# Kernel optimization log

Hardware: AMD Instinct MI355X
Metric: run time of the kernel (lower is better)

## Reference

```python
import jax, jax.numpy as jnp
import numpy as np

N, T, HID, H = 2, 2048, 1024, 16
D = HID // H


def setup_inputs() -> dict:
    key = jax.random.key(0)
    ks = jax.random.split(key, 11)
    s = 1.0 / np.sqrt(HID)
    return {
        "q": jax.random.normal(ks[0], (N, T, HID), jnp.float32),
        "k": jax.random.normal(ks[1], (N, T, HID), jnp.float32),
        "v": jax.random.normal(ks[2], (N, T, HID), jnp.float32),
        "Wq": jax.random.normal(ks[3], (HID, HID), jnp.float32) * s,
        "bq": jnp.zeros((HID,), jnp.float32),
        "Wk": jax.random.normal(ks[4], (HID, HID), jnp.float32) * s,
        "bk": jnp.zeros((HID,), jnp.float32),
        "Wv": jax.random.normal(ks[5], (HID, HID), jnp.float32) * s,
        "bv": jnp.zeros((HID,), jnp.float32),
        "Wo": jax.random.normal(ks[6], (HID, HID), jnp.float32) * s,
        "bo": jnp.zeros((HID,), jnp.float32),
    }


def reference(q, k, v, Wq, bq, Wk, bk, Wv, bv, Wo, bo):
    n, t, _ = q.shape
    # Linear projections, then the original's quirky head split:
    # .view(N, H, T, D) directly from (N, T, H*D) (no transpose).
    qh = (q @ Wq + bq).reshape(n, H, t, D)
    kh = (k @ Wk + bk).reshape(n, H, t, D)
    vh = (v @ Wv + bv).reshape(n, H, t, D)
    # scores: (N, H, T, T), scaled by sqrt(hidden_size) (not head dim)
    scores = jnp.einsum("nhtd,nhsd->nhts", qh, kh) / jnp.sqrt(jnp.float32(HID))
    # faithful quirk: softmax over dim=1 (the head axis)
    attn = jax.nn.softmax(scores, axis=1)
    # dropout is identity (eval / drop_rate=0)
    out = jnp.einsum("nhts,nhsd->nhtd", attn, vh).reshape(n, t, H * D)
    return out @ Wo + bo
```

## Files before the change

kernel.cpp:

```cpp
#include <hip/hip_runtime.h>

typedef unsigned short u16;
typedef __bf16 bf16x8 __attribute__((ext_vector_type(8)));
typedef float f32x4 __attribute__((ext_vector_type(4)));

#define MFMA16 __builtin_amdgcn_mfma_f32_16x16x32_bf16

constexpr int NB = 2, TS = 2048, HD = 1024, NH = 16, DH = 64;
constexpr float ALPHA = 0.045084220027780106f;

__device__ __forceinline__ u16 f2bf(float f) {
    union { float f; unsigned u; } v; v.f = f;
    unsigned r = v.u + 0x7FFFu + ((v.u >> 16) & 1u);
    return (u16)(r >> 16);
}
__device__ __forceinline__ float bf2f(u16 h) {
    union { unsigned u; float f; } v; v.u = ((unsigned)h) << 16;
    return v.f;
}
__device__ __forceinline__ bf16x8 ldb8(const u16* p) {
    return *reinterpret_cast<const bf16x8*>(p);
}
__device__ __forceinline__ void glds16(const u16* g, u16* l) {
    __builtin_amdgcn_global_load_lds(
        (const __attribute__((address_space(1))) unsigned int*)g,
        (__attribute__((address_space(3))) unsigned int*)l, 16, 0, 0);
}

#if defined(__has_builtin)
#  if __has_builtin(__builtin_amdgcn_cvt_pk_bf16_f32)
#    define HAVE_PKBF16 1
#  endif
#  if __has_builtin(__builtin_amdgcn_exp2f)
#    define HAVE_EXP2 1
#  endif
#endif
#ifndef HAVE_PKBF16
#  define HAVE_PKBF16 0
#endif
#ifndef HAVE_EXP2
#  define HAVE_EXP2 0
#endif
__device__ __forceinline__ unsigned pk2(float a, float b) {
#if HAVE_PKBF16
    typedef __bf16 bf16x2 __attribute__((ext_vector_type(2)));
    bf16x2 r = __builtin_amdgcn_cvt_pk_bf16_f32(a, b);
    return __builtin_bit_cast(unsigned, r);
#else
    return (unsigned)f2bf(a) | ((unsigned)f2bf(b) << 16);
#endif
}
__device__ __forceinline__ float fexp2(float x) {
#if HAVE_EXP2
    return __builtin_amdgcn_exp2f(x);
#else
    return exp2f(x);
#endif
}

__global__ __launch_bounds__(256) void to_bf16(
    const float* __restrict__ a0, const float* __restrict__ a1, const float* __restrict__ a2,
    u16* __restrict__ o0, u16* __restrict__ o1, u16* __restrict__ o2)
{
    const float* s; u16* d;
    if (blockIdx.y == 0)      { s = a0; d = o0; }
    else if (blockIdx.y == 1) { s = a1; d = o1; }
    else                      { s = a2; d = o2; }
    size_t i = ((size_t)blockIdx.x * 256 + threadIdx.x) * 8;
    float4 v0 = *reinterpret_cast<const float4*>(s + i);
    float4 v1 = *reinterpret_cast<const float4*>(s + i + 4);
    uint4 w = { pk2(v0.x, v0.y), pk2(v0.z, v0.w), pk2(v1.x, v1.y), pk2(v1.z, v1.w) };
    *reinterpret_cast<uint4*>(d + i) = w;
}

__global__ __launch_bounds__(256) void wtrans(
    const float* __restrict__ w0, const float* __restrict__ w1,
    const float* __restrict__ w2, const float* __restrict__ w3,
    u16* __restrict__ o0, u16* __restrict__ o1,
    u16* __restrict__ o2, u16* __restrict__ o3)
{
    const float* src; u16* dst; float sc;
    if (blockIdx.z == 0)      { src = w0; dst = o0; sc = ALPHA; }
    else if (blockIdx.z == 1) { src = w1; dst = o1; sc = 1.0f; }
    else if (blockIdx.z == 2) { src = w2; dst = o2; sc = 1.0f; }
    else                      { src = w3; dst = o3; sc = 1.0f; }
    __shared__ __align__(16) u16 tile[64 * 72];
    const int k0 = blockIdx.y * 64, n0 = blockIdx.x * 64;
    const int t = threadIdx.x, r = t >> 2, c0 = (t & 3) << 4;
#pragma unroll
    for (int j = 0; j < 4; ++j) {
        float4 v = *reinterpret_cast<const float4*>(&src[(size_t)(k0 + r) * HD + n0 + c0 + 4 * j]);
        tile[(c0 + 4 * j + 0) * 72 + r] = f2bf(v.x * sc);
        tile[(c0 + 4 * j + 1) * 72 + r] = f2bf(v.y * sc);
        tile[(c0 + 4 * j + 2) * 72 + r] = f2bf(v.z * sc);
        tile[(c0 + 4 * j + 3) * 72 + r] = f2bf(v.w * sc);
    }
    __syncthreads();
#pragma unroll
    for (int j = 0; j < 2; ++j)
        *reinterpret_cast<uint4*>(&dst[(size_t)(n0 + r) * HD + k0 + c0 + 8 * j]) =
            *reinterpret_cast<const uint4*>(&tile[r * 72 + c0 + 8 * j]);
}

__global__ __launch_bounds__(256) void gemm_qkv(
    const u16* __restrict__ A0, const u16* __restrict__ A1, const u16* __restrict__ A2,
    const u16* __restrict__ B0, const u16* __restrict__ B1, const u16* __restrict__ B2,
    const float* __restrict__ c0, const float* __restrict__ c1, const float* __restrict__ c2,
    u16* __restrict__ C0, u16* __restrict__ C1, u16* __restrict__ VT)
{
    const u16 *A, *BT; const float* bias;
    if (blockIdx.z == 0)      { A = A0; BT = B0; bias = c0; }
    else if (blockIdx.z == 1) { A = A1; BT = B1; bias = c1; }
    else                      { A = A2; BT = B2; bias = c2; }
    constexpr int N = HD, K = HD;
    __shared__ __align__(16) u16 As[128 * 32];
    __shared__ __align__(16) u16 Bs[128 * 32];
    const int m0 = blockIdx.y * 128, n0 = blockIdx.x * 128;
    const int tid = threadIdx.x, wid = tid >> 6, lane = tid & 63;
    const int q = lane >> 4, c = lane & 15;
    const int wm = wid >> 1, wn = wid & 1;
    const int srow = tid >> 2, scol = (tid & 3) << 3;
    f32x4 acc[4][4] = {};
    for (int k0 = 0; k0 < K; k0 += 32) {
        glds16(&A[(size_t)(m0 + srow) * K + k0 + scol],       &As[tid * 8]);
        glds16(&A[(size_t)(m0 + 64 + srow) * K + k0 + scol],  &As[2048 + tid * 8]);
        glds16(&BT[(size_t)(n0 + srow) * K + k0 + scol],      &Bs[tid * 8]);
        glds16(&BT[(size_t)(n0 + 64 + srow) * K + k0 + scol], &Bs[2048 + tid * 8]);
        __syncthreads();
        bf16x8 af[4], bf[4];
#pragma unroll
        for (int i = 0; i < 4; ++i)  af[i] = ldb8(&As[(wm * 64 + i * 16 + c) * 32 + q * 8]);
#pragma unroll
        for (int jn = 0; jn < 4; ++jn) bf[jn] = ldb8(&Bs[(wn * 64 + jn * 16 + c) * 32 + q * 8]);
#pragma unroll
        for (int i = 0; i < 4; ++i)
#pragma unroll
            for (int jn = 0; jn < 4; ++jn)
                acc[i][jn] = MFMA16(bf[jn], af[i], acc[i][jn], 0, 0, 0);
        __syncthreads();
    }
    if (blockIdx.z == 2) {
#pragma unroll
        for (int i = 0; i < 4; ++i)
#pragma unroll
            for (int jn = 0; jn < 4; ++jn) {
                int row = m0 + wm * 64 + i * 16 + c;
                int nn = row >> 11, tp = row & 2047;
                int col = n0 + wn * 64 + jn * 16 + q * 4;
                int hh  = tp >> 7;
                int tau = ((tp & 127) << 4) + (col >> 6);
                int d0  = col & 63;
#pragma unroll
                for (int r = 0; r < 4; ++r)
                    VT[(size_t)((nn * 16 + hh) * 64 + d0 + r) * 2048 + tau] =
                        f2bf(acc[i][jn][r] + bias[col + r]);
            }
    } else {
        u16* C = (blockIdx.z == 0) ? C0 : C1;
        const float bsc = (blockIdx.z == 0) ? ALPHA : 1.0f;
#pragma unroll
        for (int i = 0; i < 4; ++i)
#pragma unroll
            for (int jn = 0; jn < 4; ++jn) {
                int row = m0 + wm * 64 + i * 16 + c;
                int col = n0 + wn * 64 + jn * 16 + q * 4;
                float4 bb = *reinterpret_cast<const float4*>(&bias[col]);
                uint2 w = { pk2(acc[i][jn][0] + bb.x * bsc, acc[i][jn][1] + bb.y * bsc),
                            pk2(acc[i][jn][2] + bb.z * bsc, acc[i][jn][3] + bb.w * bsc) };
                *reinterpret_cast<uint2*>(&C[(size_t)row * N + col]) = w;
            }
    }
}

__global__ __launch_bounds__(256) void gemm_out(
    const u16* __restrict__ A, const u16* __restrict__ BT,
    const float* __restrict__ bias, float* __restrict__ C,
    int M, int N, int K)
{
    __shared__ __align__(16) u16 As[64 * 32];
    __shared__ __align__(16) u16 Bs[128 * 32];
    const int m0 = blockIdx.y * 64, n0 = blockIdx.x * 128;
    const int tid = threadIdx.x, wid = tid >> 6, lane = tid & 63;
    const int q = lane >> 4, c = lane & 15;
    const int wm = wid >> 1, wn = wid & 1;
    const int arow = tid >> 2, acol = (tid & 3) << 3;
    f32x4 acc[2][4] = {};
    for (int k0 = 0; k0 < K; k0 += 32) {
        glds16(&A[(size_t)(m0 + arow) * K + k0 + acol], &As[tid * 8]);
        glds16(&BT[(size_t)(n0 + arow) * K + k0 + acol], &Bs[tid * 8]);
        glds16(&BT[(size_t)(n0 + 64 + arow) * K + k0 + acol], &Bs[2048 + tid * 8]);
        __syncthreads();
        bf16x8 af[2], bf[4];
#pragma unroll
        for (int jm = 0; jm < 2; ++jm) af[jm] = ldb8(&As[(wm * 32 + jm * 16 + c) * 32 + q * 8]);
#pragma unroll
        for (int jn = 0; jn < 4; ++jn) bf[jn] = ldb8(&Bs[(wn * 64 + jn * 16 + c) * 32 + q * 8]);
#pragma unroll
        for (int jm = 0; jm < 2; ++jm)
#pragma unroll
            for (int jn = 0; jn < 4; ++jn)
                acc[jm][jn] = MFMA16(bf[jn], af[jm], acc[jm][jn], 0, 0, 0);
        __syncthreads();
    }
#pragma unroll
    for (int jm = 0; jm < 2; ++jm)
#pragma unroll
        for (int jn = 0; jn < 4; ++jn) {
            int row = m0 + wm * 32 + jm * 16 + c;
            int col = n0 + wn * 64 + jn * 16 + q * 4;
            float4 bb = *reinterpret_cast<const float4*>(&bias[col]);
            float4 v = { acc[jm][jn][0] + bb.x, acc[jm][jn][1] + bb.y,
                         acc[jm][jn][2] + bb.z, acc[jm][jn][3] + bb.w };
            *reinterpret_cast<float4*>(&C[(size_t)row * N + col]) = v;
        }
}

__global__ __launch_bounds__(256) void z_kernel(
    const u16* __restrict__ Qp, const u16* __restrict__ Kp, u16* __restrict__ Zf)
{
    __shared__ __align__(16) u16 Ks[64 * 64];
    __shared__ __align__(16) u16 Qs[128 * 64];
    const int sb = blockIdx.x, tb = blockIdx.y, n = blockIdx.z;
    const int s0 = sb * 64, t0 = tb * 128;
    const int tid = threadIdx.x, wid = tid >> 6, lane = tid & 63;
    const int q = lane >> 4, c = lane & 15;
    const int krow = tid >> 3, kch = tid & 7;
    float zacc[2][4][4] = {};
    for (int h = 0; h < NH; ++h) {
        const u16* Qh = Qp + (size_t)(n * NH + h) * TS * DH;
        const u16* Kh = Kp + (size_t)(n * NH + h) * TS * DH;
        glds16(&Kh[(size_t)(s0 + krow) * DH + ((kch ^ (krow & 7)) << 3)], &Ks[tid * 8]);
        glds16(&Kh[(size_t)(s0 + 32 + krow) * DH + ((kch ^ (krow & 7)) << 3)], &Ks[2048 + tid * 8]);
#pragma unroll
        for (int L = 0; L < 4; ++L)
            glds16(&Qh[(size_t)(t0 + L * 32 + krow) * DH + ((kch ^ (krow & 7)) << 3)],
                   &Qs[L * 2048 + tid * 8]);
        __syncthreads();
        bf16x8 qa[2][2], kb[4][2];
#pragma unroll
        for (int jm = 0; jm < 2; ++jm)
#pragma unroll
            for (int kf = 0; kf < 2; ++kf)
                qa[jm][kf] = ldb8(&Qs[(wid * 32 + jm * 16 + c) * 64 + (((kf * 4 + q) ^ (c & 7)) << 3)]);
#pragma unroll
        for (int i = 0; i < 4; ++i)
#pragma unroll
            for (int kf = 0; kf < 2; ++kf)
                kb[i][kf] = ldb8(&Ks[(i * 16 + c) * 64 + (((kf * 4 + q) ^ (c & 7)) << 3)]);
        f32x4 s_[2][4] = {};
#pragma unroll
        for (int kf = 0; kf < 2; ++kf)
#pragma unroll
            for (int jm = 0; jm < 2; ++jm)
#pragma unroll
                for (int i = 0; i < 4; ++i)
                    s_[jm][i] = MFMA16(kb[i][kf], qa[jm][kf], s_[jm][i], 0, 0, 0);
#pragma unroll
        for (int jm = 0; jm < 2; ++jm)
#pragma unroll
            for (int i = 0; i < 4; ++i)
#pragma unroll
                for (int r = 0; r < 4; ++r)
                    zacc[jm][i][r] += fexp2(s_[jm][i][r]);
        __syncthreads();
    }
#pragma unroll
    for (int jm = 0; jm < 2; ++jm) {
        int t = t0 + wid * 32 + jm * 16 + c;
        size_t zb = ((size_t)((n * 32 + sb) * 2048) + t) * 64 + q * 16;
        unsigned w32[8];
#pragma unroll
        for (int i = 0; i < 4; ++i) {
            w32[i * 2 + 0] = pk2(1.0f / zacc[jm][i][0], 1.0f / zacc[jm][i][1]);
            w32[i * 2 + 1] = pk2(1.0f / zacc[jm][i][2], 1.0f / zacc[jm][i][3]);
        }
        *reinterpret_cast<uint4*>(&Zf[zb])     = *reinterpret_cast<const uint4*>(&w32[0]);
        *reinterpret_cast<uint4*>(&Zf[zb + 8]) = *reinterpret_cast<const uint4*>(&w32[4]);
    }
}

__global__ __launch_bounds__(256) void attn_kernel(
    const u16* __restrict__ Qp, const u16* __restrict__ Kp, const u16* __restrict__ VT,
    const u16* __restrict__ Zf, u16* __restrict__ o2)
{
    __shared__ __align__(16) u16 Ks[64 * 64];
    __shared__ __align__(16) u16 Vs[64 * 64];
    __shared__ __align__(16) u16 Ps[64 * 72];
    const int tb = blockIdx.x, h = blockIdx.y, n = blockIdx.z;
    const int t0 = tb * 64;
    const int tid = threadIdx.x, wid = tid >> 6, lane = tid & 63;
    const int q = lane >> 4, c = lane & 15;
    const int krow = tid >> 3, kch = tid & 7;
    const size_t base = (size_t)(n * NH + h) * TS * DH;
    const u16* Qh = Qp + base; const u16* Kh = Kp + base; const u16* VTh = VT + base;
    const int tme = t0 + wid * 16 + c;
    bf16x8 qa[2];
#pragma unroll
    for (int kf = 0; kf < 2; ++kf)
        qa[kf] = ldb8(&Qh[(size_t)tme * DH + kf * 32 + q * 8]);
    f32x4 oacc[4] = {};
    for (int sb = 0; sb < 32; ++sb) {
        const int s0 = sb * 64;
        glds16(&Kh[(size_t)(s0 + krow) * DH + ((kch ^ (krow & 7)) << 3)], &Ks[tid * 8]);
        glds16(&Kh[(size_t)(s0 + 32 + krow) * DH + ((kch ^ (krow & 7)) << 3)], &Ks[2048 + tid * 8]);
        glds16(&VTh[(size_t)krow * TS + s0 + ((kch ^ (krow & 7)) << 3)], &Vs[tid * 8]);
        glds16(&VTh[(size_t)(32 + krow) * TS + s0 + ((kch ^ (krow & 7)) << 3)], &Vs[2048 + tid * 8]);
        size_t zb = ((size_t)((n * 32 + sb) * 2048) + tme) * 64 + q * 16;
        u16 zl[16];
        *reinterpret_cast<uint4*>(&zl[0]) = *reinterpret_cast<const uint4*>(&Zf[zb]);
        *reinterpret_cast<uint4*>(&zl[8]) = *reinterpret_cast<const uint4*>(&Zf[zb + 8]);
        __syncthreads();
        bf16x8 kb[4][2];
#pragma unroll
        for (int i = 0; i < 4; ++i)
#pragma unroll
            for (int kf = 0; kf < 2; ++kf)
                kb[i][kf] = ldb8(&Ks[(i * 16 + c) * 64 + (((kf * 4 + q) ^ (c & 7)) << 3)]);
        f32x4 s_[4] = {};
#pragma unroll
        for (int kf = 0; kf < 2; ++kf)
#pragma unroll
            for (int i = 0; i < 4; ++i)
                s_[i] = MFMA16(kb[i][kf], qa[kf], s_[i], 0, 0, 0);
#pragma unroll
        for (int i = 0; i < 4; ++i) {
            float p0 = fexp2(s_[i][0]) * bf2f(zl[i * 4 + 0]);
            float p1 = fexp2(s_[i][1]) * bf2f(zl[i * 4 + 1]);
            float p2 = fexp2(s_[i][2]) * bf2f(zl[i * 4 + 2]);
            float p3 = fexp2(s_[i][3]) * bf2f(zl[i * 4 + 3]);
            uint2 w = { pk2(p0, p1), pk2(p2, p3) };
            *reinterpret_cast<uint2*>(&Ps[(wid * 16 + c) * 72 + i * 16 + q * 4]) = w;
        }
        bf16x8 pa[2], vb[4][2];
#pragma unroll
        for (int kf = 0; kf < 2; ++kf)
            pa[kf] = ldb8(&Ps[(wid * 16 + c) * 72 + kf * 32 + q * 8]);
#pragma unroll
        for (int dn = 0; dn < 4; ++dn)
#pragma unroll
            for (int kf = 0; kf < 2; ++kf)
                vb[dn][kf] = ldb8(&Vs[(dn * 16 + c) * 64 + (((kf * 4 + q) ^ (c & 7)) << 3)]);
#pragma unroll
        for (int kf = 0; kf < 2; ++kf)
#pragma unroll
            for (int dn = 0; dn < 4; ++dn)
                oacc[dn] = MFMA16(vb[dn][kf], pa[kf], oacc[dn], 0, 0, 0);
        __syncthreads();
    }
#pragma unroll
    for (int dn = 0; dn < 4; ++dn) {
        uint2 w = { pk2(oacc[dn][0], oacc[dn][1]), pk2(oacc[dn][2], oacc[dn][3]) };
        *reinterpret_cast<uint2*>(&o2[base + (size_t)tme * DH + dn * 16 + q * 4]) = w;
    }
}

extern "C" void kernel_launch(void* const* d_in, const int* in_sizes, int n_in,
                              void* d_out, int out_size, void* d_ws, size_t ws_size,
                              hipStream_t stream)
{
    const float* q  = (const float*)d_in[0];
    const float* k  = (const float*)d_in[1];
    const float* v  = (const float*)d_in[2];
    const float* Wq = (const float*)d_in[3];
    const float* bq = (const float*)d_in[4];
    const float* Wk = (const float*)d_in[5];
    const float* bk = (const float*)d_in[6];
    const float* Wv = (const float*)d_in[7];
    const float* bv = (const float*)d_in[8];
    const float* Wo = (const float*)d_in[9];
    const float* bo = (const float*)d_in[10];
    float* out = (float*)d_out;

    u16* ws  = (u16*)d_ws;
    u16* wqT = ws + 0 * 1048576;
    u16* wkT = ws + 1 * 1048576;
    u16* wvT = ws + 2 * 1048576;
    u16* woT = ws + 3 * 1048576;
    u16* S1  = ws + 4194304;
    u16* S2  = S1 + 4194304;
    u16* S3  = S2 + 4194304;
    u16* S4  = S3 + 4194304;
    u16* S5  = S4 + 4194304;
    u16* S6  = S5 + 4194304;
    u16 *qb = S1, *kb = S2, *vb = S3;
    u16 *Qp = S4, *Kp = S5, *VTb = S6;
    u16 *Zf = S1, *o2 = S3;

    to_bf16<<<dim3(2048, 3), 256, 0, stream>>>(q, k, v, qb, kb, vb);
    wtrans<<<dim3(16, 16, 4), 256, 0, stream>>>(Wq, Wk, Wv, Wo, wqT, wkT, wvT, woT);
    gemm_qkv<<<dim3(8, 32, 3), 256, 0, stream>>>(qb, kb, vb, wqT, wkT, wvT,
                                                 bq, bk, bv, Qp, Kp, VTb);
    z_kernel<<<dim3(32, 16, 2), 256, 0, stream>>>(Qp, Kp, Zf);
    attn_kernel<<<dim3(32, 16, 2), 256, 0, stream>>>(Qp, Kp, VTb, Zf, o2);
    gemm_out<<<dim3(8, 64), 256, 0, stream>>>(o2, woT, bo, out, NB * TS, HD, HD);
}
```

Measured before the change: 304.1 us.

## Replace scattered V-transpose epilogue with coalesced store plus separate LDS transpose kernel

The QKV GEMM no longer writes V transposed with scattered 2-byte stores. It now writes V row-major with packed stores like Q and K, and a new vtrans kernel transposes V per head through shared memory with 16-byte accesses. Global pointer arithmetic in the GEMM, z and attention loops is also strength-reduced to incrementing pointers. This removes uncoalesced writes at the cost of one extra kernel launch and an extra read and write pass over V.

Measured after the change: 295.4 us. 1.03x faster.

```diff
diff --git a/kernel.cpp b/kernel.cpp
--- a/kernel.cpp
+++ b/kernel.cpp
@@ -106,12 +106,12 @@
     const u16* __restrict__ A0, const u16* __restrict__ A1, const u16* __restrict__ A2,
     const u16* __restrict__ B0, const u16* __restrict__ B1, const u16* __restrict__ B2,
     const float* __restrict__ c0, const float* __restrict__ c1, const float* __restrict__ c2,
-    u16* __restrict__ C0, u16* __restrict__ C1, u16* __restrict__ VT)
-{
-    const u16 *A, *BT; const float* bias;
-    if (blockIdx.z == 0)      { A = A0; BT = B0; bias = c0; }
-    else if (blockIdx.z == 1) { A = A1; BT = B1; bias = c1; }
-    else                      { A = A2; BT = B2; bias = c2; }
+    u16* __restrict__ C0, u16* __restrict__ C1, u16* __restrict__ C2)
+{
+    const u16 *A, *BT; const float* bias; u16* C; float bsc;
+    if (blockIdx.z == 0)      { A = A0; BT = B0; bias = c0; C = C0; bsc = ALPHA; }
+    else if (blockIdx.z == 1) { A = A1; BT = B1; bias = c1; C = C1; bsc = 1.0f; }
+    else                      { A = A2; BT = B2; bias = c2; C = C2; bsc = 1.0f; }
     constexpr int N = HD, K = HD;
     __shared__ __align__(16) u16 As[128 * 32];
     __shared__ __align__(16) u16 Bs[128 * 32];
@@ -120,12 +120,17 @@
     const int q = lane >> 4, c = lane & 15;
     const int wm = wid >> 1, wn = wid & 1;
     const int srow = tid >> 2, scol = (tid & 3) << 3;
+    const u16* ag0 = A + (size_t)(m0 + srow) * K + scol;
+    const u16* ag1 = A + (size_t)(m0 + 64 + srow) * K + scol;
+    const u16* bg0 = BT + (size_t)(n0 + srow) * K + scol;
+    const u16* bg1 = BT + (size_t)(n0 + 64 + srow) * K + scol;
     f32x4 acc[4][4] = {};
     for (int k0 = 0; k0 < K; k0 += 32) {
-        glds16(&A[(size_t)(m0 + srow) * K + k0 + scol],       &As[tid * 8]);
-        glds16(&A[(size_t)(m0 + 64 + srow) * K + k0 + scol],  &As[2048 + tid * 8]);
-        glds16(&BT[(size_t)(n0 + srow) * K + k0 + scol],      &Bs[tid * 8]);
-        glds16(&BT[(size_t)(n0 + 64 + srow) * K + k0 + scol], &Bs[2048 + tid * 8]);
+        glds16(ag0, &As[tid * 8]);
+        glds16(ag1, &As[2048 + tid * 8]);
+        glds16(bg0, &Bs[tid * 8]);
+        glds16(bg1, &Bs[2048 + tid * 8]);
+        ag0 += 32; ag1 += 32; bg0 += 32; bg1 += 32;
         __syncthreads();
         bf16x8 af[4], bf[4];
 #pragma unroll
@@ -139,37 +144,37 @@
                 acc[i][jn] = MFMA16(bf[jn], af[i], acc[i][jn], 0, 0, 0);
         __syncthreads();
     }
-    if (blockIdx.z == 2) {
-#pragma unroll
-        for (int i = 0; i < 4; ++i)
-#pragma unroll
-            for (int jn = 0; jn < 4; ++jn) {
-                int row = m0 + wm * 64 + i * 16 + c;
-                int nn = row >> 11, tp = row & 2047;
-                int col = n0 + wn * 64 + jn * 16 + q * 4;
-                int hh  = tp >> 7;
-                int tau = ((tp & 127) << 4) + (col >> 6);
-                int d0  = col & 63;
-#pragma unroll
-                for (int r = 0; r < 4; ++r)
-                    VT[(size_t)((nn * 16 + hh) * 64 + d0 + r) * 2048 + tau] =
-                        f2bf(acc[i][jn][r] + bias[col + r]);
-            }
-    } else {
-        u16* C = (blockIdx.z == 0) ? C0 : C1;
-        const float bsc = (blockIdx.z == 0) ? ALPHA : 1.0f;
-#pragma unroll
-        for (int i = 0; i < 4; ++i)
-#pragma unroll
-            for (int jn = 0; jn < 4; ++jn) {
-                int row = m0 + wm * 64 + i * 16 + c;
-                int col = n0 + wn * 64 + jn * 16 + q * 4;
-                float4 bb = *reinterpret_cast<const float4*>(&bias[col]);
-                uint2 w = { pk2(acc[i][jn][0] + bb.x * bsc, acc[i][jn][1] + bb.y * bsc),
-                            pk2(acc[i][jn][2] + bb.z * bsc, acc[i][jn][3] + bb.w * bsc) };
-                *reinterpret_cast<uint2*>(&C[(size_t)row * N + col]) = w;
-            }
-    }
+#pragma unroll
+    for (int i = 0; i < 4; ++i)
+#pragma unroll
+        for (int jn = 0; jn < 4; ++jn) {
+            int row = m0 + wm * 64 + i * 16 + c;
+            int col = n0 + wn * 64 + jn * 16 + q * 4;
+            float4 bb = *reinterpret_cast<const float4*>(&bias[col]);
+            uint2 w = { pk2(acc[i][jn][0] + bb.x * bsc, acc[i][jn][1] + bb.y * bsc),
+                        pk2(acc[i][jn][2] + bb.z * bsc, acc[i][jn][3] + bb.w * bsc) };
+            *reinterpret_cast<uint2*>(&C[(size_t)row * N + col]) = w;
+        }
+}
+
+__global__ __launch_bounds__(256) void vtrans(const u16* __restrict__ V, u16* __restrict__ VT)
+{
+    __shared__ __align__(16) u16 tile[64 * 72];
+    const int nh = blockIdx.y, t0 = blockIdx.x * 64;
+    const u16* src = V + (size_t)nh * TS * DH;
+    u16* dst = VT + (size_t)nh * DH * TS;
+    const int t = threadIdx.x, r = t >> 2, c0 = (t & 3) << 4;
+    *reinterpret_cast<uint4*>(&tile[r * 72 + c0]) =
+        *reinterpret_cast<const uint4*>(&src[(size_t)(t0 + r) * DH + c0]);
+    *reinterpret_cast<uint4*>(&tile[r * 72 + c0 + 8]) =
+        *reinterpret_cast<const uint4*>(&src[(size_t)(t0 + r) * DH + c0 + 8]);
+    __syncthreads();
+    const int d = t >> 2, tc = (t & 3) << 4;
+    u16 tmp[16];
+#pragma unroll
+    for (int j = 0; j < 16; ++j) tmp[j] = tile[(tc + j) * 72 + d];
+    *reinterpret_cast<uint4*>(&dst[(size_t)d * TS + t0 + tc]) = *reinterpret_cast<const uint4*>(&tmp[0]);
+    *reinterpret_cast<uint4*>(&dst[(size_t)d * TS + t0 + tc + 8]) = *reinterpret_cast<const uint4*>(&tmp[8]);
 }
 
 __global__ __launch_bounds__(256) void gemm_out(
@@ -184,11 +189,15 @@
     const int q = lane >> 4, c = lane & 15;
     const int wm = wid >> 1, wn = wid & 1;
     const int arow = tid >> 2, acol = (tid & 3) << 3;
+    const u16* ag = A + (size_t)(m0 + arow) * K + acol;
+    const u16* bg0 = BT + (size_t)(n0 + arow) * K + acol;
+    const u16* bg1 = BT + (size_t)(n0 + 64 + arow) * K + acol;
     f32x4 acc[2][4] = {};
     for (int k0 = 0; k0 < K; k0 += 32) {
-        glds16(&A[(size_t)(m0 + arow) * K + k0 + acol], &As[tid * 8]);
-        glds16(&BT[(size_t)(n0 + arow) * K + k0 + acol], &Bs[tid * 8]);
-        glds16(&BT[(size_t)(n0 + 64 + arow) * K + k0 + acol], &Bs[2048 + tid * 8]);
+        glds16(ag, &As[tid * 8]);
+        glds16(bg0, &Bs[tid * 8]);
+        glds16(bg1, &Bs[2048 + tid * 8]);
+        ag += 32; bg0 += 32; bg1 += 32;
         __syncthreads();
         bf16x8 af[2], bf[4];
 #pragma unroll
@@ -225,16 +234,17 @@
     const int tid = threadIdx.x, wid = tid >> 6, lane = tid & 63;
     const int q = lane >> 4, c = lane & 15;
     const int krow = tid >> 3, kch = tid & 7;
+    const int xsw = (kch ^ (krow & 7)) << 3;
+    const u16* kg0 = Kp + (size_t)(n * NH) * TS * DH + (size_t)(s0 + krow) * DH + xsw;
+    const u16* qg0 = Qp + (size_t)(n * NH) * TS * DH + (size_t)(t0 + krow) * DH + xsw;
     float zacc[2][4][4] = {};
     for (int h = 0; h < NH; ++h) {
-        const u16* Qh = Qp + (size_t)(n * NH + h) * TS * DH;
-        const u16* Kh = Kp + (size_t)(n * NH + h) * TS * DH;
-        glds16(&Kh[(size_t)(s0 + krow) * DH + ((kch ^ (krow & 7)) << 3)], &Ks[tid * 8]);
-        glds16(&Kh[(size_t)(s0 + 32 + krow) * DH + ((kch ^ (krow & 7)) << 3)], &Ks[2048 + tid * 8]);
+        glds16(kg0, &Ks[tid * 8]);
+        glds16(kg0 + (size_t)32 * DH, &Ks[2048 + tid * 8]);
 #pragma unroll
         for (int L = 0; L < 4; ++L)
-            glds16(&Qh[(size_t)(t0 + L * 32 + krow) * DH + ((kch ^ (krow & 7)) << 3)],
-                   &Qs[L * 2048 + tid * 8]);
+            glds16(qg0 + (size_t)(L * 32) * DH, &Qs[L * 2048 + tid * 8]);
+        kg0 += (size_t)TS * DH; qg0 += (size_t)TS * DH;
         __syncthreads();
         bf16x8 qa[2][2], kb[4][2];
 #pragma unroll
@@ -291,24 +301,29 @@
     const int tid = threadIdx.x, wid = tid >> 6, lane = tid & 63;
     const int q = lane >> 4, c = lane & 15;
     const int krow = tid >> 3, kch = tid & 7;
+    const int xsw = (kch ^ (krow & 7)) << 3;
     const size_t base = (size_t)(n * NH + h) * TS * DH;
-    const u16* Qh = Qp + base; const u16* Kh = Kp + base; const u16* VTh = VT + base;
+    const u16* Qh = Qp + base;
     const int tme = t0 + wid * 16 + c;
     bf16x8 qa[2];
 #pragma unroll
     for (int kf = 0; kf < 2; ++kf)
         qa[kf] = ldb8(&Qh[(size_t)tme * DH + kf * 32 + q * 8]);
+    const u16* kg0 = Kp + base + (size_t)krow * DH + xsw;
+    const u16* kg1 = kg0 + (size_t)32 * DH;
+    const u16* vg0 = VT + base + (size_t)krow * TS + xsw;
+    const u16* vg1 = vg0 + (size_t)32 * TS;
+    const u16* zg  = Zf + ((size_t)(n * 32) * 2048 + tme) * 64 + q * 16;
     f32x4 oacc[4] = {};
     for (int sb = 0; sb < 32; ++sb) {
-        const int s0 = sb * 64;
-        glds16(&Kh[(size_t)(s0 + krow) * DH + ((kch ^ (krow & 7)) << 3)], &Ks[tid * 8]);
-        glds16(&Kh[(size_t)(s0 + 32 + krow) * DH + ((kch ^ (krow & 7)) << 3)], &Ks[2048 + tid * 8]);
-        glds16(&VTh[(size_t)krow * TS + s0 + ((kch ^ (krow & 7)) << 3)], &Vs[tid * 8]);
-        glds16(&VTh[(size_t)(32 + krow) * TS + s0 + ((kch ^ (krow & 7)) << 3)], &Vs[2048 + tid * 8]);
-        size_t zb = ((size_t)((n * 32 + sb) * 2048) + tme) * 64 + q * 16;
+        glds16(kg0, &Ks[tid * 8]);
+        glds16(kg1, &Ks[2048 + tid * 8]);
+        glds16(vg0, &Vs[tid * 8]);
+        glds16(vg1, &Vs[2048 + tid * 8]);
         u16 zl[16];
-        *reinterpret_cast<uint4*>(&zl[0]) = *reinterpret_cast<const uint4*>(&Zf[zb]);
-        *reinterpret_cast<uint4*>(&zl[8]) = *reinterpret_cast<const uint4*>(&Zf[zb + 8]);
+        *reinterpret_cast<uint4*>(&zl[0]) = *reinterpret_cast<const uint4*>(zg);
+        *reinterpret_cast<uint4*>(&zl[8]) = *reinterpret_cast<const uint4*>(zg + 8);
+        kg0 += 64 * DH; kg1 += 64 * DH; vg0 += 64; vg1 += 64; zg += (size_t)2048 * 64;
         __syncthreads();
         bf16x8 kb[4][2];
 #pragma unroll
@@ -383,13 +398,14 @@
     u16* S5  = S4 + 4194304;
     u16* S6  = S5 + 4194304;
     u16 *qb = S1, *kb = S2, *vb = S3;
-    u16 *Qp = S4, *Kp = S5, *VTb = S6;
-    u16 *Zf = S1, *o2 = S3;
+    u16 *Qp = S4, *Kp = S5, *Vp = S6;
+    u16 *VTb = S1, *Zf = S2, *o2 = S6;
 
     to_bf16<<<dim3(2048, 3), 256, 0, stream>>>(q, k, v, qb, kb, vb);
     wtrans<<<dim3(16, 16, 4), 256, 0, stream>>>(Wq, Wk, Wv, Wo, wqT, wkT, wvT, woT);
     gemm_qkv<<<dim3(8, 32, 3), 256, 0, stream>>>(qb, kb, vb, wqT, wkT, wvT,
-                                                 bq, bk, bv, Qp, Kp, VTb);
+                                                 bq, bk, bv, Qp, Kp, Vp);
+    vtrans<<<dim3(32, 32), 256, 0, stream>>>(Vp, VTb);
     z_kernel<<<dim3(32, 16, 2), 256, 0, stream>>>(Qp, Kp, Zf);
     attn_kernel<<<dim3(32, 16, 2), 256, 0, stream>>>(Qp, Kp, VTb, Zf, o2);
     gemm_out<<<dim3(8, 64), 256, 0, stream>>>(o2, woT, bo, out, NB * TS, HD, HD);
```
